# Kernel tuning notes

Measured on AMD Instinct MI355X. Metric: run time of the kernel, lower is better.

Reference implementation:

```python
import jax, jax.numpy as jnp
import numpy as np

D_MODEL = 2048
N_HEADS = 16
HEAD_DIM = 128
WINDOW = 256
B, T = 2, 2048
SCALE = float(np.sqrt(HEAD_DIM))


def setup_inputs() -> dict:
    key = jax.random.key(0)
    ks = jax.random.split(key, 5)
    init = 0.02
    x = jax.random.normal(ks[0], (B, T, D_MODEL), dtype=jnp.float32)
    Wq = jax.random.normal(ks[1], (D_MODEL, D_MODEL), dtype=jnp.float32) * init
    Wk = jax.random.normal(ks[2], (D_MODEL, D_MODEL), dtype=jnp.float32) * init
    Wv = jax.random.normal(ks[3], (D_MODEL, D_MODEL), dtype=jnp.float32) * init
    Wo = jax.random.normal(ks[4], (D_MODEL, D_MODEL), dtype=jnp.float32) * init
    return {"x": x, "Wq": Wq, "Wk": Wk, "Wv": Wv, "Wo": Wo}


def _allowed_mask():
    # [H, T, T] bool: global (even) heads -> causal; local (odd) heads -> causal band of WINDOW
    idx = jnp.arange(T)
    causal = idx[None, :] <= idx[:, None]                      # [T, T]
    band = idx[None, :] >= (idx[:, None] - WINDOW + 1)         # [T, T]
    is_global = (jnp.arange(N_HEADS) % 2) == 0                 # [H]
    return causal[None] & (is_global[:, None, None] | band[None])


def reference(x, Wq, Wk, Wv, Wo):
    # projections (nn.Linear: y = x @ W.T), reshape to [B, H, T, D]
    def proj(W):
        return (x @ W.T).reshape(B, T, N_HEADS, HEAD_DIM).transpose(0, 2, 1, 3)

    q, k, v = proj(Wq), proj(Wk), proj(Wv)
    scores = jnp.einsum("bhtd,bhsd->bhts", q, k) / SCALE       # [B, H, T, T]
    allowed = _allowed_mask()                                  # [H, T, T]
    neg_inf = jnp.asarray(-jnp.inf, dtype=scores.dtype)
    scores = jnp.where(allowed[None], scores, neg_inf)
    attn = jax.nn.softmax(scores, axis=-1)
    out = jnp.einsum("bhts,bhsd->bhtd", attn, v)               # [B, H, T, D]
    concat = out.transpose(0, 2, 1, 3).reshape(B, T, N_HEADS * HEAD_DIM)
    return concat @ Wo.T
```

## Files before the change

### kernel.cpp

```cpp
#include <hip/hip_runtime.h>

typedef __attribute__((ext_vector_type(4))) float f32x4;
typedef __attribute__((ext_vector_type(8))) short bf16x8;
typedef __attribute__((ext_vector_type(4))) unsigned short u16x4;
typedef unsigned short u16;

#define MFMA16(a, b, c) __builtin_amdgcn_mfma_f32_16x16x32_bf16((a), (b), (c), 0, 0, 0)

#define T_SEQ 2048
#define DMODEL 2048
#define NHEADS 16
#define HDIM 128
#define WINDOW 256
#define MROWS 4096
#define SC 0.08838834764831845f

__device__ __forceinline__ u16 f2bf(float f) {
  union { float f; unsigned u; } v; v.f = f;
  return (u16)((v.u + 0x7FFFu + ((v.u >> 16) & 1u)) >> 16);
}
__device__ __forceinline__ float bf2f(u16 u) {
  union { unsigned u; float f; } v; v.u = ((unsigned)u) << 16;
  return v.f;
}
__device__ __forceinline__ void gl_lds16(const u16* g, u16* l) {
  __builtin_amdgcn_global_load_lds((const __attribute__((address_space(1))) void*)(g),
                                   (__attribute__((address_space(3))) void*)(l), 16, 0, 0);
}

#define BAR __builtin_amdgcn_s_barrier()
#define FEN asm volatile("" ::: "memory")
#define VMC6 asm volatile("s_waitcnt vmcnt(6)" ::: "memory")
#define VMC4 asm volatile("s_waitcnt vmcnt(4)" ::: "memory")
#define VMC0 asm volatile("s_waitcnt vmcnt(0)" ::: "memory")

__global__ __launch_bounds__(256) void convert_all(const float* __restrict__ x,
                                                   const float* __restrict__ wq,
                                                   const float* __restrict__ wk,
                                                   const float* __restrict__ wv,
                                                   const float* __restrict__ wo,
                                                   u16* __restrict__ dst) {
  const size_t NX = (size_t)MROWS * DMODEL;
  const size_t NW = (size_t)DMODEL * DMODEL;
  const size_t chunks = (NX + 4 * NW) / 8;
  for (size_t ci = (size_t)blockIdx.x * 256 + threadIdx.x; ci < chunks;
       ci += (size_t)gridDim.x * 256) {
    const size_t off = ci * 8;
    const float* src;
    size_t so;
    if (off < NX) { src = x; so = off; }
    else {
      size_t rem = off - NX;
      if (rem < NW) { src = wq; so = rem; }
      else if (rem < 2 * NW) { src = wk; so = rem - NW; }
      else if (rem < 3 * NW) { src = wv; so = rem - 2 * NW; }
      else { src = wo; so = rem - 3 * NW; }
    }
    f32x4 a = *(const f32x4*)&src[so];
    f32x4 b = *(const f32x4*)&src[so + 4];
    bf16x8 o;
#pragma unroll
    for (int j = 0; j < 4; ++j) { o[j] = (short)f2bf(a[j]); o[j + 4] = (short)f2bf(b[j]); }
    *(bf16x8*)&dst[off] = o;
  }
}

__global__ __launch_bounds__(256, 2) void gemm_qkv(const u16* __restrict__ A,
                                                   const u16* __restrict__ W,
                                                   u16* __restrict__ qb,
                                                   u16* __restrict__ kb,
                                                   u16* __restrict__ vb) {
  __shared__ u16 lds[40960];
  const int tid = threadIdx.x, w = tid >> 6, lane = tid & 63;
  const int fr = lane & 15, g = lane >> 4, g4 = g * 4;
  const int xk = fr & 7;

  const int xcd = blockIdx.x & 7, bi = blockIdx.x >> 3;
  const int mt = bi >> 2, nt = xcd * 4 + (bi & 3);
  const int m0 = mt * 128, n0 = nt * 192;

  const int xs0 = (g ^ xk) * 8;
  const int xs1 = xs0 ^ 32;
  const int bRow = w * 48 + fr;

  const u16* pA[4];
  const u16* pB[6];
#pragma unroll
  for (int j = 0; j < 4; ++j) {
    const int gi = j * 256 + tid, row = gi >> 3, ch = (gi & 7) ^ (row & 7);
    pA[j] = A + (size_t)(m0 + row) * DMODEL + ch * 8;
  }
#pragma unroll
  for (int j = 0; j < 6; ++j) {
    const int gi = j * 256 + tid, row = gi >> 3, ch = (gi & 7) ^ (row & 7);
    pB[j] = W + (size_t)(n0 + row) * DMODEL + ch * 8;
  }

#define SA(t, c)                                                                       \
  { _Pragma("unroll") for (int j = 0; j < 4; ++j)                                      \
      gl_lds16(pA[j] + (size_t)(t) * 64, &lds[(c) * 8192 + j * 2048 + w * 512]); }
#define SB(t, c)                                                                       \
  { _Pragma("unroll") for (int j = 0; j < 6; ++j)                                      \
      gl_lds16(pB[j] + (size_t)(t) * 64, &lds[16384 + (c) * 12288 + j * 2048 + w * 512]); }

#define RD_AL(c)                                                                       \
  { _Pragma("unroll") for (int m_ = 0; m_ < 4; ++m_) {                                 \
      af[m_][0] = *(const bf16x8*)&lds[(c) * 8192 + (fr + m_ * 16) * 64 + xs0];        \
      af[m_][1] = *(const bf16x8*)&lds[(c) * 8192 + (fr + m_ * 16) * 64 + xs1]; } }
#define RD_AH(c)                                                                       \
  { _Pragma("unroll") for (int m_ = 0; m_ < 4; ++m_) {                                 \
      af[m_][0] = *(const bf16x8*)&lds[(c) * 8192 + (fr + 64 + m_ * 16) * 64 + xs0];   \
      af[m_][1] = *(const bf16x8*)&lds[(c) * 8192 + (fr + 64 + m_ * 16) * 64 + xs1]; } }
#define RD_B(c)                                                                        \
  { _Pragma("unroll") for (int n_ = 0; n_ < 3; ++n_) {                                 \
      bfr[n_][0] = *(const bf16x8*)&lds[16384 + (c) * 12288 + (bRow + n_ * 16) * 64 + xs0]; \
      bfr[n_][1] = *(const bf16x8*)&lds[16384 + (c) * 12288 + (bRow + n_ * 16) * 64 + xs1]; } }

#define MMQ(MB)                                                                        \
  { __builtin_amdgcn_s_setprio(1);                                                    \
    _Pragma("unroll") for (int kc_ = 0; kc_ < 2; ++kc_)                                \
      _Pragma("unroll") for (int m_ = 0; m_ < 4; ++m_)                                 \
        _Pragma("unroll") for (int n_ = 0; n_ < 3; ++n_)                               \
          acc[(MB) + m_][n_] = MFMA16(af[m_][kc_], bfr[n_][kc_], acc[(MB) + m_][n_]);  \
    __builtin_amdgcn_s_setprio(0); }

  bf16x8 af[4][2], bfr[3][2];
  f32x4 acc[8][3];
#pragma unroll
  for (int i = 0; i < 8; ++i)
#pragma unroll
    for (int j = 0; j < 3; ++j) acc[i][j] = (f32x4){0.f, 0.f, 0.f, 0.f};

  SA(0, 0); SB(0, 0);
  SB(1, 1);
  VMC6; BAR;

#pragma unroll 1
  for (int i = 0; i < 15; ++i) {
    const int t0 = 2 * i;
    RD_AL(0); RD_B(0); SA(t0 + 1, 1);
    FEN; BAR; MMQ(0); FEN; BAR;
    RD_AH(0); SB(t0 + 2, 0);
    VMC6; BAR; MMQ(4); FEN; BAR;
    RD_AL(1); RD_B(1); SA(t0 + 2, 0);
    FEN; BAR; MMQ(0); FEN; BAR;
    RD_AH(1); SB(t0 + 3, 1);
    VMC6; BAR; MMQ(4); FEN; BAR;
  }
  RD_AL(0); RD_B(0); SA(31, 1);
  FEN; BAR; MMQ(0); FEN; BAR;
  RD_AH(0);
  VMC0; BAR; MMQ(4); FEN; BAR;
  RD_AL(1); RD_B(1);
  FEN; BAR; MMQ(0); FEN; BAR;
  RD_AH(1);
  FEN; BAR; MMQ(4);

#pragma unroll
  for (int mi = 0; mi < 8; ++mi)
#pragma unroll
    for (int ni = 0; ni < 3; ++ni) {
      const int row0 = m0 + mi * 16 + g4;
      const int cg = n0 + w * 48 + ni * 16 + fr;
      const int bb = row0 >> 11, tl = row0 & 2047;
      if (cg < DMODEL) {
#pragma unroll
        for (int r = 0; r < 4; ++r)
          qb[(size_t)(row0 + r) * DMODEL + cg] = f2bf(acc[mi][ni][r] * SC);
      } else if (cg < 2 * DMODEL) {
        const int cc = cg - DMODEL;
        const int hh = cc >> 7, d = cc & 127;
        const size_t kbase = (size_t)(bb * NHEADS + hh) * T_SEQ * HDIM;
#pragma unroll
        for (int r = 0; r < 4; ++r)
          kb[kbase + (size_t)(tl + r) * HDIM + d] = f2bf(acc[mi][ni][r]);
      } else {
        const int cc = cg - 2 * DMODEL;
        const int hh = cc >> 7, d = cc & 127;
        u16x4 w4;
#pragma unroll
        for (int r = 0; r < 4; ++r) w4[r] = f2bf(acc[mi][ni][r]);
        *(u16x4*)&vb[(size_t)(bb * NHEADS + hh) * T_SEQ * HDIM + (size_t)(tl >> 6) * 8192 +
                     d * 64 + (tl & 63)] = w4;
      }
    }
#undef SA
#undef SB
#undef RD_AL
#undef RD_AH
#undef RD_B
#undef MMQ
}

__global__ __launch_bounds__(256, 2) void gemm_out(const u16* __restrict__ A,
                                                   const u16* __restrict__ W0,
                                                   float* __restrict__ outf) {
  __shared__ u16 lds2[32768];
  const int tid = threadIdx.x, w = tid >> 6, lane = tid & 63;
  const int fr = lane & 15, g = lane >> 4, g4 = g * 4;
  const int xk = fr & 7;

  const int xcd = blockIdx.x & 7, bi = blockIdx.x >> 3;
  const int mt = bi >> 1, nt = xcd * 2 + (bi & 1);
  const int m0 = mt * 128, n0 = nt * 128;

  const int xs0 = (g ^ xk) * 8;
  const int xs1 = xs0 ^ 32;
  const int bRow = w * 32 + fr;

  const u16* pA[4];
  const u16* pB[4];
#pragma unroll
  for (int j = 0; j < 4; ++j) {
    const int gi = j * 256 + tid, row = gi >> 3, ch = (gi & 7) ^ (row & 7);
    pA[j] = A + (size_t)(m0 + row) * DMODEL + ch * 8;
    pB[j] = W0 + (size_t)(n0 + row) * DMODEL + ch * 8;
  }

#define S2A(t, c)                                                                      \
  { _Pragma("unroll") for (int j = 0; j < 4; ++j)                                      \
      gl_lds16(pA[j] + (size_t)(t) * 64, &lds2[(c) * 8192 + j * 2048 + w * 512]); }
#define S2B(t, c)                                                                      \
  { _Pragma("unroll") for (int j = 0; j < 4; ++j)                                      \
      gl_lds16(pB[j] + (size_t)(t) * 64, &lds2[16384 + (c) * 8192 + j * 2048 + w * 512]); }

#define R2AL(c)                                                                        \
  { _Pragma("unroll") for (int m_ = 0; m_ < 4; ++m_) {                                 \
      af[m_][0] = *(const bf16x8*)&lds2[(c) * 8192 + (fr + m_ * 16) * 64 + xs0];       \
      af[m_][1] = *(const bf16x8*)&lds2[(c) * 8192 + (fr + m_ * 16) * 64 + xs1]; } }
#define R2AH(c)                                                                        \
  { _Pragma("unroll") for (int m_ = 0; m_ < 4; ++m_) {                                 \
      af[m_][0] = *(const bf16x8*)&lds2[(c) * 8192 + (fr + 64 + m_ * 16) * 64 + xs0];  \
      af[m_][1] = *(const bf16x8*)&lds2[(c) * 8192 + (fr + 64 + m_ * 16) * 64 + xs1]; } }
#define R2B(c)                                                                         \
  { _Pragma("unroll") for (int n_ = 0; n_ < 2; ++n_) {                                 \
      bfr[n_][0] = *(const bf16x8*)&lds2[16384 + (c) * 8192 + (bRow + n_ * 16) * 64 + xs0]; \
      bfr[n_][1] = *(const bf16x8*)&lds2[16384 + (c) * 8192 + (bRow + n_ * 16) * 64 + xs1]; } }

#define M2(MB)                                                                         \
  { __builtin_amdgcn_s_setprio(1);                                                    \
    _Pragma("unroll") for (int kc_ = 0; kc_ < 2; ++kc_)                                \
      _Pragma("unroll") for (int m_ = 0; m_ < 4; ++m_)                                 \
        _Pragma("unroll") for (int n_ = 0; n_ < 2; ++n_)                               \
          acc[(MB) + m_][n_] = MFMA16(af[m_][kc_], bfr[n_][kc_], acc[(MB) + m_][n_]);  \
    __builtin_amdgcn_s_setprio(0); }

  bf16x8 af[4][2], bfr[2][2];
  f32x4 acc[8][2];
#pragma unroll
  for (int i = 0; i < 8; ++i)
#pragma unroll
    for (int j = 0; j < 2; ++j) acc[i][j] = (f32x4){0.f, 0.f, 0.f, 0.f};

  S2A(0, 0); S2B(0, 0);
  S2B(1, 1);
  VMC4; BAR;

#pragma unroll 1
  for (int i = 0; i < 15; ++i) {
    const int t0 = 2 * i;
    R2AL(0); R2B(0); S2A(t0 + 1, 1);
    FEN; BAR; M2(0); FEN; BAR;
    R2AH(0); S2B(t0 + 2, 0);
    VMC4; BAR; M2(4); FEN; BAR;
    R2AL(1); R2B(1); S2A(t0 + 2, 0);
    FEN; BAR; M2(0); FEN; BAR;
    R2AH(1); S2B(t0 + 3, 1);
    VMC4; BAR; M2(4); FEN; BAR;
  }
  R2AL(0); R2B(0); S2A(31, 1);
  FEN; BAR; M2(0); FEN; BAR;
  R2AH(0);
  VMC0; BAR; M2(4); FEN; BAR;
  R2AL(1); R2B(1);
  FEN; BAR; M2(0); FEN; BAR;
  R2AH(1);
  FEN; BAR; M2(4);

#pragma unroll
  for (int mi = 0; mi < 8; ++mi)
#pragma unroll
    for (int ni = 0; ni < 2; ++ni) {
      const int row0 = m0 + mi * 16 + g4;
      const int c = n0 + w * 32 + ni * 16 + fr;
#pragma unroll
      for (int r = 0; r < 4; ++r)
        outf[(size_t)(row0 + r) * DMODEL + c] = acc[mi][ni][r];
    }
#undef S2A
#undef S2B
#undef R2AL
#undef R2AH
#undef R2B
#undef M2
}

#define QB 128
#define KVB 64

__global__ __launch_bounds__(512, 4) void attn_kernel(const u16* __restrict__ qb,
                                                      const u16* __restrict__ kb,
                                                      const u16* __restrict__ vb,
                                                      u16* __restrict__ op,
                                                      u16* __restrict__ pO,
                                                      float* __restrict__ pm,
                                                      float* __restrict__ pl) {
  __shared__ u16 lds[40960];

  const int xcdid = blockIdx.x & 7, j = blockIdx.x >> 3;
  const int p = xcdid * 4 + j / 24;
  const int bx = j % 24;
  const int h = p & 15, b = p >> 4;

  const bool isglobal = (h & 1) == 0;
  int qt, klo, khi, part = 0;
  bool partial = false;
  if (isglobal) {
    if (bx < 16) {
      qt = 15 - (bx >> 1);
      part = bx & 1;
      partial = true;
      if (part == 0) { klo = 0; khi = 15; } else { klo = 16; khi = 2 * qt + 1; }
    } else {
      qt = 23 - bx;
      klo = 0; khi = 2 * qt + 1;
    }
  } else {
    if (bx >= 16) return;
    qt = 15 - bx;
    const int lo_ = qt * QB - (WINDOW - 1);
    klo = lo_ > 0 ? (lo_ >> 6) : 0;
    khi = 2 * qt + 1;
  }

  const int tid = threadIdx.x, wave = tid >> 6, lane = tid & 63;
  const int fr = lane & 15, g = lane >> 4, g4 = g * 4;
  const int xk = fr & 7;
  const int q0 = qt * QB;
  const int bh = b * NHEADS + h;
  const size_t basek = (size_t)bh * T_SEQ * HDIM;
  const size_t baseo = (size_t)b * T_SEQ * DMODEL + (size_t)h * HDIM;

  bf16x8 qf[4];
  {
    const int qrow = q0 + wave * 16 + fr;
#pragma unroll
    for (int ds = 0; ds < 4; ++ds)
      qf[ds] = *(const bf16x8*)&qb[(size_t)b * T_SEQ * DMODEL + (size_t)qrow * DMODEL +
                                   (size_t)h * HDIM + ds * 32 + g * 8];
  }

  float mrun = -1e30f, lrun = 0.f;
  f32x4 o[8];
#pragma unroll
  for (int dt = 0; dt < 8; ++dt) o[dt] = (f32x4){0.f, 0.f, 0.f, 0.f};

  const int j0 = wave * 2, j1 = wave * 2 + 1;
  const int gi0 = j0 * 64 + lane, gi1 = j1 * 64 + lane;
  const int kr0 = gi0 >> 4, kc0 = (gi0 & 15) ^ (kr0 & 7);
  const int kr1 = gi1 >> 4, kc1 = (gi1 & 15) ^ (kr1 & 7);
  const u16* pK0 = kb + basek + (size_t)kr0 * HDIM + kc0 * 8;
  const u16* pK1 = kb + basek + (size_t)kr1 * HDIM + kc1 * 8;
  const int d0 = gi0 >> 3, vs0 = (gi0 & 7) ^ (d0 & 7);
  const int d1 = gi1 >> 3, vs1 = (gi1 & 7) ^ (d1 & 7);
  const u16* pV0 = vb + basek + (size_t)d0 * 64 + vs0 * 8;
  const u16* pV1 = vb + basek + (size_t)d1 * 64 + vs1 * 8;

#define STAGE(KT, c)                                                                   \
  { gl_lds16(pK0 + (size_t)(KT) * 8192, &lds[(c) * 8192 + j0 * 512]);                  \
    gl_lds16(pK1 + (size_t)(KT) * 8192, &lds[(c) * 8192 + j1 * 512]);                  \
    gl_lds16(pV0 + (size_t)(KT) * 8192, &lds[16384 + (c) * 8192 + j0 * 512]);          \
    gl_lds16(pV1 + (size_t)(KT) * 8192, &lds[16384 + (c) * 8192 + j1 * 512]); }

  u16* Pw = &lds[32768 + wave * 1024];
  const int qg = q0 + wave * 16 + fr;

  STAGE(klo, klo & 1);
  VMC0; BAR;

  for (int kt = klo; kt <= khi; ++kt) {
    const int c = kt & 1;
    const bool more = kt < khi;
    if (more) STAGE(kt + 1, c ^ 1);
    const u16* Kc = &lds[c * 8192];
    const u16* Vc = &lds[16384 + c * 8192];

    f32x4 s[4];
    __builtin_amdgcn_s_setprio(1);
#pragma unroll
    for (int kk = 0; kk < 4; ++kk) {
      f32x4 a = (f32x4){0.f, 0.f, 0.f, 0.f};
#pragma unroll
      for (int ds = 0; ds < 4; ++ds) {
        const int r = kk * 16 + fr;
        bf16x8 kf = *(const bf16x8*)&Kc[r * 128 + (((ds * 4 + g) ^ xk) << 3)];
        a = MFMA16(kf, qf[ds], a);
      }
      s[kk] = a;
    }
    __builtin_amdgcn_s_setprio(0);

    float sv[16];
    float pmax = -1e30f;
#pragma unroll
    for (int kk = 0; kk < 4; ++kk)
#pragma unroll
      for (int reg = 0; reg < 4; ++reg) {
        const int cg = kt * KVB + kk * 16 + g4 + reg;
        const bool allowed = (cg <= qg) && (isglobal || cg >= qg - (WINDOW - 1));
        const float v = allowed ? s[kk][reg] : -1e30f;
        sv[kk * 4 + reg] = v;
        pmax = fmaxf(pmax, v);
      }
    pmax = fmaxf(pmax, __shfl_xor(pmax, 16, 64));
    pmax = fmaxf(pmax, __shfl_xor(pmax, 32, 64));
    const bool resc = !__all(pmax - mrun <= 8.0f);
    float fac = 1.f;
    if (resc) {
      const float nm = fmaxf(mrun, pmax);
      fac = __expf(mrun - nm);
      mrun = nm;
    }
    float rs = 0.f;
    u16 pb[16];
#pragma unroll
    for (int i = 0; i < 16; ++i) {
      const float p_ = (sv[i] > -5e29f) ? __expf(sv[i] - mrun) : 0.f;
      rs += p_;
      pb[i] = f2bf(p_);
    }
    rs += __shfl_xor(rs, 16, 64);
    rs += __shfl_xor(rs, 32, 64);
    lrun = lrun * fac + rs;

#pragma unroll
    for (int kk = 0; kk < 4; ++kk) {
      u16x4 wv;
      wv[0] = pb[kk * 4]; wv[1] = pb[kk * 4 + 1]; wv[2] = pb[kk * 4 + 2]; wv[3] = pb[kk * 4 + 3];
      *(u16x4*)&Pw[fr * 64 + (((2 * kk + (g >> 1)) ^ xk) << 3) + (g & 1) * 4] = wv;
    }

    if (resc) {
      float ff[4];
#pragma unroll
      for (int r = 0; r < 4; ++r) ff[r] = __shfl(fac, g4 + r, 64);
#pragma unroll
      for (int dt = 0; dt < 8; ++dt)
#pragma unroll
        for (int r = 0; r < 4; ++r) o[dt][r] *= ff[r];
    }

    bf16x8 pf0 = *(const bf16x8*)&Pw[fr * 64 + ((g ^ xk) << 3)];
    bf16x8 pf1 = *(const bf16x8*)&Pw[fr * 64 + (((4 + g) ^ xk) << 3)];
    __builtin_amdgcn_s_setprio(1);
#pragma unroll
    for (int dt = 0; dt < 8; ++dt) {
      const int d = dt * 16 + fr;
      bf16x8 vf0 = *(const bf16x8*)&Vc[d * 64 + ((g ^ xk) << 3)];
      bf16x8 vf1 = *(const bf16x8*)&Vc[d * 64 + (((4 + g) ^ xk) << 3)];
      o[dt] = MFMA16(pf0, vf0, o[dt]);
      o[dt] = MFMA16(pf1, vf1, o[dt]);
    }
    __builtin_amdgcn_s_setprio(0);

    FEN;
    VMC0;
    BAR;
  }

  if (!partial) {
    const float inv = 1.0f / lrun;
    float iv[4];
#pragma unroll
    for (int r = 0; r < 4; ++r) iv[r] = __shfl(inv, g4 + r, 64);
#pragma unroll
    for (int r = 0; r < 4; ++r) {
      const int qrow = q0 + wave * 16 + g4 + r;
#pragma unroll
      for (int dt = 0; dt < 8; ++dt)
        op[baseo + (size_t)qrow * DMODEL + dt * 16 + fr] = f2bf(o[dt][r] * iv[r]);
    }
  } else {
    const int sidx = (((b * 8 + (h >> 1)) * 8 + (qt - 8)) << 1) + part;
    const size_t sb = (size_t)sidx * QB;
#pragma unroll
    for (int r = 0; r < 4; ++r) {
      const size_t row = sb + wave * 16 + g4 + r;
#pragma unroll
      for (int dt = 0; dt < 8; ++dt)
        pO[row * HDIM + dt * 16 + fr] = f2bf(o[dt][r]);
    }
    if (lane < 16) {
      pm[sb + wave * 16 + lane] = mrun;
      pl[sb + wave * 16 + lane] = lrun;
    }
  }
#undef STAGE
}

__global__ __launch_bounds__(256) void merge_kernel(const u16* __restrict__ pO,
                                                    const float* __restrict__ pm,
                                                    const float* __restrict__ pl,
                                                    u16* __restrict__ op) {
  const int x = blockIdx.x;
  const int qt8 = x & 7, eh = (x >> 3) & 7, b = x >> 6;
  const int h = eh * 2, qt = 8 + qt8;
  const int s0 = x * 2, s1 = s0 + 1;

  for (int i = 0; i < 8; ++i) {
    const int vidx = threadIdx.x + i * 256;
    const int row = vidx >> 4, d8 = (vidx & 15) * 8;
    const float m0 = pm[s0 * QB + row], m1 = pm[s1 * QB + row];
    const float l0 = pl[s0 * QB + row], l1 = pl[s1 * QB + row];
    const float m = fmaxf(m0, m1);
    const float w0 = __expf(m0 - m), w1 = __expf(m1 - m);
    const float inv = 1.0f / (l0 * w0 + l1 * w1);
    bf16x8 a = *(const bf16x8*)&pO[((size_t)s0 * QB + row) * HDIM + d8];
    bf16x8 c = *(const bf16x8*)&pO[((size_t)s1 * QB + row) * HDIM + d8];
    bf16x8 r;
#pragma unroll
    for (int j = 0; j < 8; ++j)
      r[j] = (short)f2bf((bf2f((u16)a[j]) * w0 + bf2f((u16)c[j]) * w1) * inv);
    *(bf16x8*)&op[((size_t)(b * T_SEQ + qt * QB + row)) * DMODEL + h * HDIM + d8] = r;
  }
}

extern "C" void kernel_launch(void* const* d_in, const int* in_sizes, int n_in,
                              void* d_out, int out_size, void* d_ws, size_t ws_size,
                              hipStream_t stream) {
  (void)in_sizes; (void)n_in; (void)out_size; (void)ws_size;
  const float* x  = (const float*)d_in[0];
  const float* Wq = (const float*)d_in[1];
  const float* Wk = (const float*)d_in[2];
  const float* Wv = (const float*)d_in[3];
  const float* Wo = (const float*)d_in[4];

  const size_t NX = (size_t)MROWS * DMODEL;
  const size_t NW = (size_t)DMODEL * DMODEL;
  u16* ws  = (u16*)d_ws;
  u16* xb  = ws;
  u16* wqb = ws + NX;
  u16* wkb = wqb + NW;
  u16* wvb = wkb + NW;
  u16* wob = wvb + NW;
  u16* qbb = wob + NW;
  u16* kbb = qbb + NX;
  u16* vbb = kbb + NX;

  u16*   pO = wqb;
  float* pm = (float*)(wqb + (size_t)256 * QB * HDIM);
  float* pl = pm + 256 * QB;

  convert_all<<<2048, 256, 0, stream>>>(x, Wq, Wk, Wv, Wo, ws);

  gemm_qkv<<<1024, 256, 0, stream>>>(xb, wqb, qbb, kbb, vbb);

  attn_kernel<<<768, 512, 0, stream>>>(qbb, kbb, vbb, xb, pO, pm, pl);

  merge_kernel<<<128, 256, 0, stream>>>(pO, pm, pl, xb);

  gemm_out<<<512, 256, 0, stream>>>(xb, wob, (float*)d_out);
}
```

Before: 211.0 us.

## Halve QKV GEMM K-tile to 32 to fit three blocks per CU

The QKV projection GEMM now stages K-slices of 32 instead of 64, halving the LDS footprint to 40 KB, and raises the launch bound from 2 to 3 blocks per CU. The LDS layout packs two rows per 64-element LDS line with a new XOR swizzle, and fragment registers shrink to one K-chunk each. The loop runs twice as many iterations, with vmcnt waits adjusted to the smaller load count. The aim is more occupancy to hide latency, at the cost of twice as many barriers per unit of MFMA work and a tighter register budget that could cause spills.

```diff
diff --git a/kernel.cpp b/kernel.cpp
--- a/kernel.cpp
+++ b/kernel.cpp
@@ -32,6 +32,7 @@
 #define FEN asm volatile("" ::: "memory")
 #define VMC6 asm volatile("s_waitcnt vmcnt(6)" ::: "memory")
 #define VMC4 asm volatile("s_waitcnt vmcnt(4)" ::: "memory")
+#define VMC3 asm volatile("s_waitcnt vmcnt(3)" ::: "memory")
 #define VMC0 asm volatile("s_waitcnt vmcnt(0)" ::: "memory")
 
 __global__ __launch_bounds__(256) void convert_all(const float* __restrict__ x,
@@ -65,66 +66,62 @@
   }
 }
 
-__global__ __launch_bounds__(256, 2) void gemm_qkv(const u16* __restrict__ A,
+__global__ __launch_bounds__(256, 3) void gemm_qkv(const u16* __restrict__ A,
                                                    const u16* __restrict__ W,
                                                    u16* __restrict__ qb,
                                                    u16* __restrict__ kb,
                                                    u16* __restrict__ vb) {
-  __shared__ u16 lds[40960];
+  __shared__ u16 lds[20480];
   const int tid = threadIdx.x, w = tid >> 6, lane = tid & 63;
   const int fr = lane & 15, g = lane >> 4, g4 = g * 4;
-  const int xk = fr & 7;
 
   const int xcd = blockIdx.x & 7, bi = blockIdx.x >> 3;
   const int mt = bi >> 2, nt = xcd * 4 + (bi & 3);
   const int m0 = mt * 128, n0 = nt * 192;
 
-  const int xs0 = (g ^ xk) * 8;
-  const int xs1 = xs0 ^ 32;
-  const int bRow = w * 48 + fr;
-
-  const u16* pA[4];
-  const u16* pB[6];
-#pragma unroll
-  for (int j = 0; j < 4; ++j) {
-    const int gi = j * 256 + tid, row = gi >> 3, ch = (gi & 7) ^ (row & 7);
-    pA[j] = A + (size_t)(m0 + row) * DMODEL + ch * 8;
-  }
-#pragma unroll
-  for (int j = 0; j < 6; ++j) {
-    const int gi = j * 256 + tid, row = gi >> 3, ch = (gi & 7) ^ (row & 7);
-    pB[j] = W + (size_t)(n0 + row) * DMODEL + ch * 8;
+  const int xsA = ((((fr & 1) * 4 + g) ^ (fr >> 1)) << 3);
+  const int frh = fr >> 1;
+
+  const u16* pA[2];
+  const u16* pB[3];
+#pragma unroll
+  for (int j = 0; j < 2; ++j) {
+    const int gi = j * 256 + tid, lr = gi >> 3, sl = gi & 7;
+    const int sub = sl ^ (lr & 7), row = lr * 2 + (sub >> 2), col = (sub & 3) * 8;
+    pA[j] = A + (size_t)(m0 + row) * DMODEL + col;
+  }
+#pragma unroll
+  for (int j = 0; j < 3; ++j) {
+    const int gi = j * 256 + tid, lr = gi >> 3, sl = gi & 7;
+    const int sub = sl ^ (lr & 7), row = lr * 2 + (sub >> 2), col = (sub & 3) * 8;
+    pB[j] = W + (size_t)(n0 + row) * DMODEL + col;
   }
 
 #define SA(t, c)                                                                       \
-  { _Pragma("unroll") for (int j = 0; j < 4; ++j)                                      \
-      gl_lds16(pA[j] + (size_t)(t) * 64, &lds[(c) * 8192 + j * 2048 + w * 512]); }
+  { _Pragma("unroll") for (int j = 0; j < 2; ++j)                                      \
+      gl_lds16(pA[j] + (t) * 32, &lds[(c) * 4096 + j * 2048 + w * 512]); }
 #define SB(t, c)                                                                       \
-  { _Pragma("unroll") for (int j = 0; j < 6; ++j)                                      \
-      gl_lds16(pB[j] + (size_t)(t) * 64, &lds[16384 + (c) * 12288 + j * 2048 + w * 512]); }
+  { _Pragma("unroll") for (int j = 0; j < 3; ++j)                                      \
+      gl_lds16(pB[j] + (t) * 32, &lds[8192 + (c) * 6144 + j * 2048 + w * 512]); }
 
 #define RD_AL(c)                                                                       \
-  { _Pragma("unroll") for (int m_ = 0; m_ < 4; ++m_) {                                 \
-      af[m_][0] = *(const bf16x8*)&lds[(c) * 8192 + (fr + m_ * 16) * 64 + xs0];        \
-      af[m_][1] = *(const bf16x8*)&lds[(c) * 8192 + (fr + m_ * 16) * 64 + xs1]; } }
+  { _Pragma("unroll") for (int m_ = 0; m_ < 4; ++m_)                                   \
+      af[m_] = *(const bf16x8*)&lds[(c) * 4096 + (frh + m_ * 8) * 64 + xsA]; }
 #define RD_AH(c)                                                                       \
-  { _Pragma("unroll") for (int m_ = 0; m_ < 4; ++m_) {                                 \
-      af[m_][0] = *(const bf16x8*)&lds[(c) * 8192 + (fr + 64 + m_ * 16) * 64 + xs0];   \
-      af[m_][1] = *(const bf16x8*)&lds[(c) * 8192 + (fr + 64 + m_ * 16) * 64 + xs1]; } }
+  { _Pragma("unroll") for (int m_ = 0; m_ < 4; ++m_)                                   \
+      af[m_] = *(const bf16x8*)&lds[(c) * 4096 + (frh + 32 + m_ * 8) * 64 + xsA]; }
 #define RD_B(c)                                                                        \
-  { _Pragma("unroll") for (int n_ = 0; n_ < 3; ++n_) {                                 \
-      bfr[n_][0] = *(const bf16x8*)&lds[16384 + (c) * 12288 + (bRow + n_ * 16) * 64 + xs0]; \
-      bfr[n_][1] = *(const bf16x8*)&lds[16384 + (c) * 12288 + (bRow + n_ * 16) * 64 + xs1]; } }
+  { _Pragma("unroll") for (int n_ = 0; n_ < 3; ++n_)                                   \
+      bfr[n_] = *(const bf16x8*)&lds[8192 + (c) * 6144 + (w * 24 + n_ * 8 + frh) * 64 + xsA]; }
 
 #define MMQ(MB)                                                                        \
   { __builtin_amdgcn_s_setprio(1);                                                    \
-    _Pragma("unroll") for (int kc_ = 0; kc_ < 2; ++kc_)                                \
-      _Pragma("unroll") for (int m_ = 0; m_ < 4; ++m_)                                 \
-        _Pragma("unroll") for (int n_ = 0; n_ < 3; ++n_)                               \
-          acc[(MB) + m_][n_] = MFMA16(af[m_][kc_], bfr[n_][kc_], acc[(MB) + m_][n_]);  \
+    _Pragma("unroll") for (int m_ = 0; m_ < 4; ++m_)                                   \
+      _Pragma("unroll") for (int n_ = 0; n_ < 3; ++n_)                                 \
+        acc[(MB) + m_][n_] = MFMA16(af[m_], bfr[n_], acc[(MB) + m_][n_]);              \
     __builtin_amdgcn_s_setprio(0); }
 
-  bf16x8 af[4][2], bfr[3][2];
+  bf16x8 af[4], bfr[3];
   f32x4 acc[8][3];
 #pragma unroll
   for (int i = 0; i < 8; ++i)
@@ -133,21 +130,21 @@
 
   SA(0, 0); SB(0, 0);
   SB(1, 1);
-  VMC6; BAR;
+  VMC3; BAR;
 
 #pragma unroll 1
-  for (int i = 0; i < 15; ++i) {
+  for (int i = 0; i < 31; ++i) {
     const int t0 = 2 * i;
     RD_AL(0); RD_B(0); SA(t0 + 1, 1);
     FEN; BAR; MMQ(0); FEN; BAR;
     RD_AH(0); SB(t0 + 2, 0);
-    VMC6; BAR; MMQ(4); FEN; BAR;
+    VMC3; BAR; MMQ(4); FEN; BAR;
     RD_AL(1); RD_B(1); SA(t0 + 2, 0);
     FEN; BAR; MMQ(0); FEN; BAR;
     RD_AH(1); SB(t0 + 3, 1);
-    VMC6; BAR; MMQ(4); FEN; BAR;
-  }
-  RD_AL(0); RD_B(0); SA(31, 1);
+    VMC3; BAR; MMQ(4); FEN; BAR;
+  }
+  RD_AL(0); RD_B(0); SA(63, 1);
   FEN; BAR; MMQ(0); FEN; BAR;
   RD_AH(0);
   VMC0; BAR; MMQ(4); FEN; BAR;
```

Measured after the change: 226.4 us. +7.3%, slower.
